# Performance work log

Measured on AMD Instinct MI355X. Metric: run time of the kernel, lower is better.

Reference implementation:

```python
import jax, jax.numpy as jnp
import numpy as np

B = 512        # graphs per batch
N_NODES = 64   # nodes per graph
IN_CH = 256
EMBED = 64
TOPK = 20
NEG_SLOPE = 0.2


def setup_inputs() -> dict:
    key = jax.random.key(0)
    ks = jax.random.split(key, 6)
    N = B * N_NODES
    x = jax.random.normal(ks[0], (N, IN_CH), dtype=jnp.float32)
    # fully-connected graph WITH self loops, per graph, sorted source-major
    src = jnp.repeat(jnp.arange(N_NODES, dtype=jnp.int32), N_NODES)  # [n*n]
    dst = jnp.tile(jnp.arange(N_NODES, dtype=jnp.int32), N_NODES)    # [n*n]
    offs = (jnp.arange(B, dtype=jnp.int32) * N_NODES)[:, None]       # [B,1]
    l = (src[None, :] + offs).reshape(-1)
    r = (dst[None, :] + offs).reshape(-1)
    edge_index = jnp.stack([l, r]).astype(jnp.int32)                 # [2, B*n*n]
    batch = jnp.repeat(jnp.arange(B, dtype=jnp.int32), N_NODES)      # [N]
    glorot = lambda k, sh: jax.random.uniform(k, sh, jnp.float32,
                                              -1.0, 1.0) * np.sqrt(6.0 / (sh[0] + sh[-1]))
    Wl = glorot(ks[1], (EMBED, IN_CH))
    bl = jnp.zeros((EMBED,), jnp.float32)
    Wr = glorot(ks[2], (EMBED, IN_CH))
    br = jnp.zeros((EMBED,), jnp.float32)
    att = glorot(ks[3], (1, EMBED))
    return {"x": x, "edge_index": edge_index, "batch": batch,
            "Wl": Wl, "bl": bl, "Wr": Wr, "br": br, "att": att}


def reference(x, edge_index, batch, Wl, bl, Wr, br, att):
    N = x.shape[0]
    x_l = x @ Wl.T + bl                      # [N, D]
    x_r = x @ Wr.T + br                      # [N, D]
    l, r = edge_index[0], edge_index[1]
    # edge gather + GAT-style score
    e = jax.nn.leaky_relu(x_l[l] + x_r[r], negative_slope=NEG_SLOPE)  # [E, D]
    alpha = (e * att[0]).sum(axis=-1)                                  # [E]
    # segment softmax grouped by source node l (each group is non-empty)
    m = jax.ops.segment_max(alpha, l, num_segments=N)
    a = jnp.exp(alpha - m[l])
    s = jax.ops.segment_sum(a, l, num_segments=N)
    a = a / s[l]
    # kNN sparsify: zero the diagonal then per-row topk
    a3 = a.reshape(B, N_NODES, N_NODES)
    a3 = a3 * (1.0 - jnp.eye(N_NODES, dtype=a3.dtype))
    attention, indices = jax.lax.top_k(a3, TOPK)     # [B, n, k] sorted desc
    attention = attention.reshape(-1)                 # [B*n*k]
    offs = (jnp.arange(B, dtype=jnp.int32) * N_NODES)[:, None]
    index_i = (jnp.repeat(jnp.arange(N_NODES, dtype=jnp.int32), TOPK)[None, :]
               + offs).reshape(-1)
    index_j = (indices.astype(jnp.int32)
               + (jnp.arange(B, dtype=jnp.int32) * N_NODES)[:, None, None]).reshape(-1)
    new_edge_index = jnp.stack([index_i, index_j])    # [2, B*n*k]
    return new_edge_index, attention
```

## Files before the change

kernel.cpp:

```cpp
#include <hip/hip_runtime.h>
#include <stdint.h>

#define NGRAPH 512
#define NN 64
#define INCH 256
#define TOPK 20
#define EPR 655360

typedef __attribute__((ext_vector_type(8))) short bf16x8;
typedef __attribute__((ext_vector_type(4))) float f32x4;

#define STG   0
#define XLR   0
#define XRR   4352
#define SMEM_DW 10240

static __device__ __forceinline__ uint32_t f2bfbits(float f) {
  uint32_t u = __float_as_uint(f);
  return (u + 0x7FFFu + ((u >> 16) & 1u)) >> 16;
}
static __device__ __forceinline__ uint32_t pk2(float a, float b) {
  return f2bfbits(a) | (f2bfbits(b) << 16);
}

static __device__ __forceinline__ float keyalpha(uint32_t k) {
  uint32_t ub = (k & 0x80000000u) ? (k ^ 0x80000000u) : ~k;
  return __uint_as_float(ub & 0xFFFFFFC0u);
}

static __device__ __forceinline__ float redsum64(float v) {
  int p;
  p = __builtin_amdgcn_update_dpp(0, __float_as_int(v), 0xB1, 0xF, 0xF, true);
  v += __int_as_float(p);
  p = __builtin_amdgcn_update_dpp(0, __float_as_int(v), 0x4E, 0xF, 0xF, true);
  v += __int_as_float(p);
  v += __shfl_xor(v, 4);
  v += __shfl_xor(v, 8);
  v += __shfl_xor(v, 16);
  v += __shfl_xor(v, 32);
  return v;
}

__global__ __launch_bounds__(256) void wpack(const float* __restrict__ Wl,
                                             const float* __restrict__ Wr,
                                             uint32_t* __restrict__ ws) {
  const int t = blockIdx.x * 256 + threadIdx.x;
  const float* src = (t < 8192) ? Wl : Wr;
  const int p = t & 8191;
  float2 v = *(const float2*)(src + (size_t)p * 2);
  ws[t] = pk2(v.x, v.y);
}

__global__ __launch_bounds__(1024, 8) void gat_fused(
    const float* __restrict__ x,
    const uint32_t* __restrict__ ws,
    const float* __restrict__ blv,
    const float* __restrict__ brv,
    const float* __restrict__ att,
    float* __restrict__ out)
{
  __shared__ __align__(16) uint32_t smemU[SMEM_DW];
  float* smemF = (float*)smemU;

  const int b    = blockIdx.x;
  const int t    = threadIdx.x;
  const int w    = t >> 6;
  const int lane = t & 63;
  const int quad = lane >> 4;
  const int lo   = lane & 15;
  const int nodeBase = b * NN;

  const int half = w >> 3;
  const int r0   = ((w >> 1) & 3) * 16;
  const int kh   = w & 1;
  const int pair = w >> 1;

  f32x4 acc[4];
  #pragma unroll
  for (int ct = 0; ct < 4; ++ct) acc[ct] = (f32x4){0.f, 0.f, 0.f, 0.f};

  const uint4* wsV = (const uint4*)ws;
  #pragma unroll
  for (int ksl = 0; ksl < 4; ++ksl) {
    const int ks = kh * 4 + ksl;
    const int k0 = ks * 32 + quad * 8;
    const float* ap = x + (size_t)(nodeBase + r0 + lo) * INCH + k0;
    float4 a0 = *(const float4*)ap;
    float4 a1 = *(const float4*)(ap + 4);
    uint4 au = { pk2(a0.x, a0.y), pk2(a0.z, a0.w), pk2(a1.x, a1.y), pk2(a1.z, a1.w) };
    bf16x8 afrag = __builtin_bit_cast(bf16x8, au);
    #pragma unroll
    for (int ct = 0; ct < 4; ++ct) {
      const int n = ct * 16 + lo;
      uint4 bu = wsV[half * 2048 + n * 32 + ks * 4 + quad];
      bf16x8 bfrag = __builtin_bit_cast(bf16x8, bu);
      acc[ct] = __builtin_amdgcn_mfma_f32_16x16x32_bf16(afrag, bfrag, acc[ct], 0, 0, 0);
    }
  }

  if (kh) {
    #pragma unroll
    for (int ct = 0; ct < 4; ++ct)
      *(f32x4*)&smemF[STG + pair * 1280 + (ct * 16 + lo) * 20 + quad * 4] = acc[ct];
  }
  __syncthreads();

  f32x4 vfin[4];
  if (!kh) {
    const float* bias = half ? brv : blv;
    #pragma unroll
    for (int ct = 0; ct < 4; ++ct) {
      f32x4 pv = *(const f32x4*)&smemF[STG + pair * 1280 + (ct * 16 + lo) * 20 + quad * 4];
      const float bb = bias[ct * 16 + lo];
      vfin[ct][0] = acc[ct][0] + pv[0] + bb;
      vfin[ct][1] = acc[ct][1] + pv[1] + bb;
      vfin[ct][2] = acc[ct][2] + pv[2] + bb;
      vfin[ct][3] = acc[ct][3] + pv[3] + bb;
    }
  }
  __syncthreads();
  if (!kh) {
    if (half == 0) {
      #pragma unroll
      for (int ct = 0; ct < 4; ++ct)
        #pragma unroll
        for (int rg = 0; rg < 4; ++rg)
          smemF[XLR + (r0 + quad * 4 + rg) * 68 + ct * 16 + lo] = vfin[ct][rg];
    } else {
      #pragma unroll
      for (int ct = 0; ct < 4; ++ct)
        #pragma unroll
        for (int rg = 0; rg < 4; ++rg) {
          const int row = r0 + quad * 4 + rg;
          const int dsw = (ct * 16 + lo) ^ ((row & 7) << 2);
          smemF[XRR + row * 64 + dsw] = vfin[ct][rg];
        }
    }
  }
  __syncthreads();

  const int rB = w * 4;

  float xlv[4];
  #pragma unroll
  for (int q = 0; q < 4; ++q)
    xlv[q] = smemF[XLR + (rB + q) * 68 + lane];

  const float attv = att[lane];
  float sl[4];
  #pragma unroll
  for (int q = 0; q < 4; ++q)
    sl[q] = redsum64(attv * xlv[q]);

  float pacc[4] = {0.f, 0.f, 0.f, 0.f};
  float srp = 0.f;
  const int xrb = XRR + lane * 64;
  const int sw  = lane & 7;
  #pragma unroll
  for (int c = 0; c < 4; ++c) {
    f32x4 xrc[4];
    #pragma unroll
    for (int g = 0; g < 4; ++g)
      xrc[g] = *(const f32x4*)&smemF[xrb + (((c * 4 + g) ^ sw) << 2)];
    #pragma unroll
    for (int dl = 0; dl < 16; ++dl) {
      const int d = c * 16 + dl;
      const float xv = xrc[dl >> 2][dl & 3];
      const float av = att[d];
      srp = fmaf(av, xv, srp);
      #pragma unroll
      for (int q = 0; q < 4; ++q) {
        const float xls = __int_as_float(
            __builtin_amdgcn_readlane(__float_as_int(xlv[q]), d));
        pacc[q] = fmaf(av, fabsf(xls + xv), pacc[q]);
      }
    }
  }

  float aq[4];
  #pragma unroll
  for (int q = 0; q < 4; ++q)
    aq[q] = 0.6f * (sl[q] + srp) + 0.4f * pacc[q];

  uint32_t key[4];
  #pragma unroll
  for (int q = 0; q < 4; ++q) {
    const uint32_t u = __float_as_uint(aq[q]);
    uint32_t kk = u ^ ((uint32_t)((int32_t)u >> 31) | 0x80000000u);
    kk = (kk & 0xFFFFFFC0u) | (uint32_t)(63 - lane);
    key[q] = (lane == rB + q) ? 0u : kk;
  }

  #pragma unroll
  for (int k = 2; k <= 64; k <<= 1) {
    #pragma unroll
    for (int j = k >> 1; j >= 1; j >>= 1) {
      const bool keep_max = (((lane & k) == 0) == ((lane & j) == 0));
      #pragma unroll
      for (int q = 0; q < 4; ++q) {
        uint32_t p;
        if (j == 1)
          p = (uint32_t)__builtin_amdgcn_update_dpp(0, (int)key[q], 0xB1, 0xF, 0xF, true);
        else if (j == 2)
          p = (uint32_t)__builtin_amdgcn_update_dpp(0, (int)key[q], 0x4E, 0xF, 0xF, true);
        else
          p = (uint32_t)__shfl_xor((int)key[q], j);
        const uint32_t mx = (key[q] > p) ? key[q] : p;
        const uint32_t mn = (key[q] > p) ? p : key[q];
        key[q] = keep_max ? mx : mn;
      }
    }
  }

  float mq[4], Sq[4];
  #pragma unroll
  for (int q = 0; q < 4; ++q) {
    const uint32_t tk = (uint32_t)__builtin_amdgcn_readlane((int)key[q], 0);
    const float topa  = keyalpha(tk);
    const float adiag = __int_as_float(
        __builtin_amdgcn_readlane(__float_as_int(aq[q]), rB + q));
    mq[q] = fmaxf(topa, adiag);
    Sq[q] = redsum64(__expf(aq[q] - mq[q]));
  }

  if (lane < TOPK) {
    #pragma unroll
    for (int q = 0; q < 4; ++q) {
      const int g = nodeBase + rB + q;
      const uint32_t kq = key[q];
      const float alpha = keyalpha(kq);
      const int jj = 63 - (int)(kq & 63u);
      const float va = __expf(alpha - mq[q]) * (1.0f / Sq[q]);
      out[(size_t)g * 20 + lane] = (float)g;
      out[(size_t)EPR + (size_t)g * 20 + lane] = (float)(nodeBase + jj);
      out[2 * (size_t)EPR + (size_t)g * 20 + lane] = va;
    }
  }
}

extern "C" void kernel_launch(void* const* d_in, const int* in_sizes, int n_in,
                              void* d_out, int out_size, void* d_ws, size_t ws_size,
                              hipStream_t stream) {
  const float* x   = (const float*)d_in[0];
  const float* Wl  = (const float*)d_in[3];
  const float* bl  = (const float*)d_in[4];
  const float* Wr  = (const float*)d_in[5];
  const float* br  = (const float*)d_in[6];
  const float* att = (const float*)d_in[7];
  uint32_t* wsW = (uint32_t*)d_ws;

  wpack<<<dim3(64), dim3(256), 0, stream>>>(Wl, Wr, wsW);
  gat_fused<<<dim3(NGRAPH), dim3(1024), 0, stream>>>(x, wsW, bl, br, att, (float*)d_out);
}
```

Measured before the change: 130.6 us.

## Pre-pack x and W into MFMA fragment order, halve block size, drop K-split

Adds an xpack pre-kernel that converts x to bf16 in MFMA fragment order inside the workspace, and repacks W so each lane's fragment loads are coalesced. The fused kernel now runs 512 threads per graph. Each wave does the full K=256 reduction, which removes the split-K partial-sum exchange and two barriers. Each wave also scores 8 rows instead of 4, and att is broadcast with readlane instead of being re-read from memory. The cost is an extra kernel launch plus a full write and re-read of x in bf16, more registers per wave, and a fallback path if the workspace is too small.

After: 124.6 us. 4.7% less time.

```diff
diff --git a/kernel.cpp b/kernel.cpp
--- a/kernel.cpp
+++ b/kernel.cpp
@@ -6,14 +6,14 @@
 #define INCH 256
 #define TOPK 20
 #define EPR 655360
+#define WS_NEED ((size_t)65536 + (size_t)16777216)
 
 typedef __attribute__((ext_vector_type(8))) short bf16x8;
 typedef __attribute__((ext_vector_type(4))) float f32x4;
 
-#define STG   0
-#define XLR   0
-#define XRR   4352
-#define SMEM_DW 10240
+#define XLR 0
+#define XRR 4352
+#define SMEM_DW 8704
 
 static __device__ __forceinline__ uint32_t f2bfbits(float f) {
   uint32_t u = __float_as_uint(f);
@@ -22,12 +22,10 @@
 static __device__ __forceinline__ uint32_t pk2(float a, float b) {
   return f2bfbits(a) | (f2bfbits(b) << 16);
 }
-
 static __device__ __forceinline__ float keyalpha(uint32_t k) {
   uint32_t ub = (k & 0x80000000u) ? (k ^ 0x80000000u) : ~k;
   return __uint_as_float(ub & 0xFFFFFFC0u);
 }
-
 static __device__ __forceinline__ float redsum64(float v) {
   int p;
   p = __builtin_amdgcn_update_dpp(0, __float_as_int(v), 0xB1, 0xF, 0xF, true);
@@ -41,19 +39,34 @@
   return v;
 }
 
-__global__ __launch_bounds__(256) void wpack(const float* __restrict__ Wl,
-                                             const float* __restrict__ Wr,
-                                             uint32_t* __restrict__ ws) {
+__global__ __launch_bounds__(256) void wpack2(const float* __restrict__ Wl,
+                                              const float* __restrict__ Wr,
+                                              uint4* __restrict__ wsW) {
   const int t = blockIdx.x * 256 + threadIdx.x;
-  const float* src = (t < 8192) ? Wl : Wr;
-  const int p = t & 8191;
-  float2 v = *(const float2*)(src + (size_t)p * 2);
-  ws[t] = pk2(v.x, v.y);
-}
-
-__global__ __launch_bounds__(1024, 8) void gat_fused(
+  const int lo = t & 15, quad = (t >> 4) & 3, ct = (t >> 6) & 3;
+  const int ks = (t >> 8) & 7, half = (t >> 11) & 1;
+  const int n = ct * 16 + lo, k0 = ks * 32 + quad * 8;
+  const float* src = half ? Wr : Wl;
+  const float4* s4 = (const float4*)(src + (size_t)n * INCH + k0);
+  float4 a0 = s4[0], a1 = s4[1];
+  wsW[t] = (uint4){ pk2(a0.x, a0.y), pk2(a0.z, a0.w), pk2(a1.x, a1.y), pk2(a1.z, a1.w) };
+}
+
+__global__ __launch_bounds__(256) void xpack(const float* __restrict__ x,
+                                             uint4* __restrict__ xp) {
+  const int t = blockIdx.x * 256 + threadIdx.x;
+  const int lo = t & 15, quad = (t >> 4) & 3, rt = (t >> 6) & 3;
+  const int ks = (t >> 8) & 7, b = t >> 11;
+  const int row = b * 64 + rt * 16 + lo, k0 = ks * 32 + quad * 8;
+  const float4* s4 = (const float4*)(x + (size_t)row * INCH + k0);
+  float4 a0 = s4[0], a1 = s4[1];
+  xp[t] = (uint4){ pk2(a0.x, a0.y), pk2(a0.z, a0.w), pk2(a1.x, a1.y), pk2(a1.z, a1.w) };
+}
+
+template <bool XP>
+__global__ __launch_bounds__(512, 4) void gat_fused(
     const float* __restrict__ x,
-    const uint32_t* __restrict__ ws,
+    const uint4* __restrict__ wsV,
     const float* __restrict__ blv,
     const float* __restrict__ brv,
     const float* __restrict__ att,
@@ -70,106 +83,85 @@
   const int lo   = lane & 15;
   const int nodeBase = b * NN;
 
-  const int half = w >> 3;
-  const int r0   = ((w >> 1) & 3) * 16;
-  const int kh   = w & 1;
-  const int pair = w >> 1;
+  const float attv = att[lane];
+
+  const int half = w >> 2;
+  const int rt   = w & 3;
+  const int r0   = rt * 16;
+  const uint4* xpV = wsV + 4096;
 
   f32x4 acc[4];
   #pragma unroll
   for (int ct = 0; ct < 4; ++ct) acc[ct] = (f32x4){0.f, 0.f, 0.f, 0.f};
 
-  const uint4* wsV = (const uint4*)ws;
-  #pragma unroll
-  for (int ksl = 0; ksl < 4; ++ksl) {
-    const int ks = kh * 4 + ksl;
-    const int k0 = ks * 32 + quad * 8;
-    const float* ap = x + (size_t)(nodeBase + r0 + lo) * INCH + k0;
-    float4 a0 = *(const float4*)ap;
-    float4 a1 = *(const float4*)(ap + 4);
-    uint4 au = { pk2(a0.x, a0.y), pk2(a0.z, a0.w), pk2(a1.x, a1.y), pk2(a1.z, a1.w) };
-    bf16x8 afrag = __builtin_bit_cast(bf16x8, au);
+  #pragma unroll
+  for (int ks = 0; ks < 8; ++ks) {
+    bf16x8 afrag;
+    if constexpr (XP) {
+      uint4 au = xpV[(size_t)b * 2048 + ks * 256 + rt * 64 + quad * 16 + lo];
+      afrag = __builtin_bit_cast(bf16x8, au);
+    } else {
+      const int k0 = ks * 32 + quad * 8;
+      const float* ap = x + (size_t)(nodeBase + r0 + lo) * INCH + k0;
+      float4 a0 = *(const float4*)ap;
+      float4 a1 = *(const float4*)(ap + 4);
+      uint4 au = { pk2(a0.x, a0.y), pk2(a0.z, a0.w), pk2(a1.x, a1.y), pk2(a1.z, a1.w) };
+      afrag = __builtin_bit_cast(bf16x8, au);
+    }
     #pragma unroll
     for (int ct = 0; ct < 4; ++ct) {
-      const int n = ct * 16 + lo;
-      uint4 bu = wsV[half * 2048 + n * 32 + ks * 4 + quad];
+      uint4 bu = wsV[half * 2048 + ks * 256 + ct * 64 + quad * 16 + lo];
       bf16x8 bfrag = __builtin_bit_cast(bf16x8, bu);
       acc[ct] = __builtin_amdgcn_mfma_f32_16x16x32_bf16(afrag, bfrag, acc[ct], 0, 0, 0);
     }
   }
 
-  if (kh) {
-    #pragma unroll
-    for (int ct = 0; ct < 4; ++ct)
-      *(f32x4*)&smemF[STG + pair * 1280 + (ct * 16 + lo) * 20 + quad * 4] = acc[ct];
+  {
+    const float* bias = half ? brv : blv;
+    const int dstBase = half ? XRR : XLR;
+    #pragma unroll
+    for (int ct = 0; ct < 4; ++ct) {
+      const int d = ct * 16 + lo;
+      const float bb = bias[d];
+      #pragma unroll
+      for (int rg = 0; rg < 4; ++rg)
+        smemF[dstBase + (r0 + quad * 4 + rg) * 68 + d] = acc[ct][rg] + bb;
+    }
   }
   __syncthreads();
 
-  f32x4 vfin[4];
-  if (!kh) {
-    const float* bias = half ? brv : blv;
-    #pragma unroll
-    for (int ct = 0; ct < 4; ++ct) {
-      f32x4 pv = *(const f32x4*)&smemF[STG + pair * 1280 + (ct * 16 + lo) * 20 + quad * 4];
-      const float bb = bias[ct * 16 + lo];
-      vfin[ct][0] = acc[ct][0] + pv[0] + bb;
-      vfin[ct][1] = acc[ct][1] + pv[1] + bb;
-      vfin[ct][2] = acc[ct][2] + pv[2] + bb;
-      vfin[ct][3] = acc[ct][3] + pv[3] + bb;
-    }
-  }
-  __syncthreads();
-  if (!kh) {
-    if (half == 0) {
-      #pragma unroll
-      for (int ct = 0; ct < 4; ++ct)
-        #pragma unroll
-        for (int rg = 0; rg < 4; ++rg)
-          smemF[XLR + (r0 + quad * 4 + rg) * 68 + ct * 16 + lo] = vfin[ct][rg];
-    } else {
-      #pragma unroll
-      for (int ct = 0; ct < 4; ++ct)
-        #pragma unroll
-        for (int rg = 0; rg < 4; ++rg) {
-          const int row = r0 + quad * 4 + rg;
-          const int dsw = (ct * 16 + lo) ^ ((row & 7) << 2);
-          smemF[XRR + row * 64 + dsw] = vfin[ct][rg];
-        }
-    }
-  }
-  __syncthreads();
-
-  const int rB = w * 4;
-
-  float xlv[4];
-  #pragma unroll
-  for (int q = 0; q < 4; ++q)
+  const int rB = w * 8;
+
+  float xlv[8];
+  #pragma unroll
+  for (int q = 0; q < 8; ++q)
     xlv[q] = smemF[XLR + (rB + q) * 68 + lane];
 
-  const float attv = att[lane];
-  float sl[4];
-  #pragma unroll
-  for (int q = 0; q < 4; ++q)
+  float sl[8];
+  #pragma unroll
+  for (int q = 0; q < 8; ++q)
     sl[q] = redsum64(attv * xlv[q]);
 
-  float pacc[4] = {0.f, 0.f, 0.f, 0.f};
+  float pacc[8];
+  #pragma unroll
+  for (int q = 0; q < 8; ++q) pacc[q] = 0.f;
   float srp = 0.f;
-  const int xrb = XRR + lane * 64;
-  const int sw  = lane & 7;
+  const int xrb = XRR + lane * 68;
   #pragma unroll
   for (int c = 0; c < 4; ++c) {
     f32x4 xrc[4];
     #pragma unroll
     for (int g = 0; g < 4; ++g)
-      xrc[g] = *(const f32x4*)&smemF[xrb + (((c * 4 + g) ^ sw) << 2)];
+      xrc[g] = *(const f32x4*)&smemF[xrb + c * 16 + g * 4];
     #pragma unroll
     for (int dl = 0; dl < 16; ++dl) {
       const int d = c * 16 + dl;
       const float xv = xrc[dl >> 2][dl & 3];
-      const float av = att[d];
+      const float av = __int_as_float(
+          __builtin_amdgcn_readlane(__float_as_int(attv), d));
       srp = fmaf(av, xv, srp);
       #pragma unroll
-      for (int q = 0; q < 4; ++q) {
+      for (int q = 0; q < 8; ++q) {
         const float xls = __int_as_float(
             __builtin_amdgcn_readlane(__float_as_int(xlv[q]), d));
         pacc[q] = fmaf(av, fabsf(xls + xv), pacc[q]);
@@ -177,14 +169,14 @@
     }
   }
 
-  float aq[4];
-  #pragma unroll
-  for (int q = 0; q < 4; ++q)
+  float aq[8];
+  #pragma unroll
+  for (int q = 0; q < 8; ++q)
     aq[q] = 0.6f * (sl[q] + srp) + 0.4f * pacc[q];
 
-  uint32_t key[4];
-  #pragma unroll
-  for (int q = 0; q < 4; ++q) {
+  uint32_t key[8];
+  #pragma unroll
+  for (int q = 0; q < 8; ++q) {
     const uint32_t u = __float_as_uint(aq[q]);
     uint32_t kk = u ^ ((uint32_t)((int32_t)u >> 31) | 0x80000000u);
     kk = (kk & 0xFFFFFFC0u) | (uint32_t)(63 - lane);
@@ -197,7 +189,7 @@
     for (int j = k >> 1; j >= 1; j >>= 1) {
       const bool keep_max = (((lane & k) == 0) == ((lane & j) == 0));
       #pragma unroll
-      for (int q = 0; q < 4; ++q) {
+      for (int q = 0; q < 8; ++q) {
         uint32_t p;
         if (j == 1)
           p = (uint32_t)__builtin_amdgcn_update_dpp(0, (int)key[q], 0xB1, 0xF, 0xF, true);
@@ -212,9 +204,9 @@
     }
   }
 
-  float mq[4], Sq[4];
-  #pragma unroll
-  for (int q = 0; q < 4; ++q) {
+  float mq[8], Sq[8];
+  #pragma unroll
+  for (int q = 0; q < 8; ++q) {
     const uint32_t tk = (uint32_t)__builtin_amdgcn_readlane((int)key[q], 0);
     const float topa  = keyalpha(tk);
     const float adiag = __int_as_float(
@@ -225,7 +217,7 @@
 
   if (lane < TOPK) {
     #pragma unroll
-    for (int q = 0; q < 4; ++q) {
+    for (int q = 0; q < 8; ++q) {
       const int g = nodeBase + rB + q;
       const uint32_t kq = key[q];
       const float alpha = keyalpha(kq);
@@ -247,8 +239,15 @@
   const float* Wr  = (const float*)d_in[5];
   const float* br  = (const float*)d_in[6];
   const float* att = (const float*)d_in[7];
-  uint32_t* wsW = (uint32_t*)d_ws;
-
-  wpack<<<dim3(64), dim3(256), 0, stream>>>(Wl, Wr, wsW);
-  gat_fused<<<dim3(NGRAPH), dim3(1024), 0, stream>>>(x, wsW, bl, br, att, (float*)d_out);
-}
+  uint4* wsW = (uint4*)d_ws;
+
+  wpack2<<<dim3(16), dim3(256), 0, stream>>>(Wl, Wr, wsW);
+  if (ws_size >= WS_NEED) {
+    xpack<<<dim3(4096), dim3(256), 0, stream>>>(x, wsW + 4096);
+    gat_fused<true><<<dim3(NGRAPH), dim3(512), 0, stream>>>(
+        x, wsW, bl, br, att, (float*)d_out);
+  } else {
+    gat_fused<false><<<dim3(NGRAPH), dim3(512), 0, stream>>>(
+        x, wsW, bl, br, att, (float*)d_out);
+  }
+}
```
